# Optimization experiments

Hardware: AMD Instinct MI355X
Metric: run time of the kernel (lower is better)

The kernel has to match this reference:

```python
import jax, jax.numpy as jnp
import numpy as np

B, C, H, W = 4, 96, 64, 64
D_STATE, D_CONV, EXPAND = 16, 4, 2
D_INNER = EXPAND * C          # 192
DT_RANK = (C + 15) // 16      # 6
BN_EPS = 1e-5


def setup_inputs() -> dict:
    key = jax.random.key(0)
    ks = jax.random.split(key, 10)
    s = 0.02
    return {
        "x": jax.random.normal(ks[0], (B, C, H, W), jnp.float32),
        # Mamba block params (mamba_ssm layout, no bias on in/out proj)
        "in_proj_w": jax.random.normal(ks[1], (2 * D_INNER, C), jnp.float32) * s,
        "conv1d_w": jax.random.normal(ks[2], (D_INNER, 1, D_CONV), jnp.float32) * s,  # depthwise
        "conv1d_b": jnp.zeros((D_INNER,), jnp.float32),
        "x_proj_w": jax.random.normal(ks[3], (DT_RANK + 2 * D_STATE, D_INNER), jnp.float32) * s,
        "dt_proj_w": jax.random.normal(ks[4], (D_INNER, DT_RANK), jnp.float32) * s,
        "dt_proj_b": jax.random.normal(ks[5], (D_INNER,), jnp.float32) * s,
        "A_log": jnp.log(jnp.tile(jnp.arange(1, D_STATE + 1, dtype=jnp.float32), (D_INNER, 1))),
        "D": jnp.ones((D_INNER,), jnp.float32),
        "out_proj_w": jax.random.normal(ks[6], (C, D_INNER), jnp.float32) * s,
        # trailing ConvBNReLU6 params
        "conv2d_w": jax.random.normal(ks[7], (C, C, 3, 3), jnp.float32) * s,
        "bn_gamma": jnp.ones((C,), jnp.float32),
        "bn_beta": jnp.zeros((C,), jnp.float32),
        "bn_mean": jnp.zeros((C,), jnp.float32),
        "bn_var": jnp.ones((C,), jnp.float32),
    }


def _forward(x, in_proj_w, conv1d_w, conv1d_b, x_proj_w, dt_proj_w, dt_proj_b,
             A_log, D, out_proj_w, conv2d_w, bn_gamma, bn_beta, bn_mean, bn_var):
    b, c, h, w = x.shape
    L = h * w
    seq = x.reshape(b, c, L).transpose(0, 2, 1)              # [B, L, C] tokens
    xz = seq @ in_proj_w.T                                    # [B, L, 2*D_INNER]
    xi, z = jnp.split(xz, 2, axis=-1)

    # depthwise causal conv1d + SiLU
    xi_c = jax.lax.conv_general_dilated(
        xi.transpose(0, 2, 1), conv1d_w, (1,), [(D_CONV - 1, 0)],
        dimension_numbers=("NCH", "OIH", "NCH"), feature_group_count=D_INNER)
    xi = jax.nn.silu((xi_c + conv1d_b[None, :, None]).transpose(0, 2, 1))  # [B, L, D_INNER]

    # input-dependent dt, B, C
    x_dbl = xi @ x_proj_w.T                                   # [B, L, DT_RANK + 2*D_STATE]
    dt, Bm, Cm = jnp.split(x_dbl, [DT_RANK, DT_RANK + D_STATE], axis=-1)
    dt = jax.nn.softplus(dt @ dt_proj_w.T + dt_proj_b)        # [B, L, D_INNER]

    # discretize: dA = exp(dt*A), dBx = dt*B*x
    A = -jnp.exp(A_log)                                       # [D_INNER, D_STATE]
    dA = jnp.exp(dt[..., None] * A)                           # [B, L, D_INNER, D_STATE]
    dBx = dt[..., None] * Bm[:, :, None, :] * xi[..., None]   # [B, L, D_INNER, D_STATE]

    def step(hst, inputs):
        dA_t, dBx_t, C_t = inputs
        hst = dA_t * hst + dBx_t                              # [B, D_INNER, D_STATE]
        y_t = jnp.einsum("bds,bs->bd", hst, C_t)
        return hst, y_t

    h0 = jnp.zeros((b, D_INNER, D_STATE), xi.dtype)
    _, ys = jax.lax.scan(step, h0,
                         (dA.transpose(1, 0, 2, 3), dBx.transpose(1, 0, 2, 3), Cm.transpose(1, 0, 2)))
    y = ys.transpose(1, 0, 2)                                 # [B, L, D_INNER]
    y = (y + xi * D) * jax.nn.silu(z)                         # skip D + gate
    out = y @ out_proj_w.T                                    # [B, L, C]
    xm = out.transpose(0, 2, 1).reshape(b, c, h, w)

    # ConvBNReLU: 3x3 conv (pad 1, no bias) -> BN (inference) -> ReLU6
    xo = jax.lax.conv_general_dilated(xm, conv2d_w, (1, 1), [(1, 1), (1, 1)],
                                      dimension_numbers=("NCHW", "OIHW", "NCHW"))
    inv = bn_gamma / jnp.sqrt(bn_var + BN_EPS)
    xo = xo * inv[None, :, None, None] + (bn_beta - bn_mean * inv)[None, :, None, None]
    return jnp.clip(xo, 0.0, 6.0)


def reference(x, in_proj_w, conv1d_w, conv1d_b, x_proj_w, dt_proj_w, dt_proj_b,
              A_log, D, out_proj_w, conv2d_w, bn_gamma, bn_beta, bn_mean, bn_var):
    return _forward(x, in_proj_w, conv1d_w, conv1d_b, x_proj_w, dt_proj_w, dt_proj_b,
                    A_log, D, out_proj_w, conv2d_w, bn_gamma, bn_beta, bn_mean, bn_var)
```

## Files before the change

### kernel.cpp

```cpp
#include <hip/hip_runtime.h>
#include <math.h>

#define LQ 4096
#define DI 192
#define DS 16
#define NCH 256
#define TCH 16

__device__ __forceinline__ float siluf_(float v) { return v / (1.f + __expf(-v)); }
__device__ __forceinline__ float softplusf_(float v) { return v > 20.f ? v : log1pf(__expf(v)); }

template <int CTRL>
__device__ __forceinline__ float dpp_shift_(float x) {
    int y = __builtin_amdgcn_update_dpp(0, __float_as_int(x), CTRL, 0xf, 0xf, true);
    return __int_as_float(y);
}
__device__ __forceinline__ void async_g2l16_(const float* g, float* l) {
    __builtin_amdgcn_global_load_lds(
        (const __attribute__((address_space(1))) void*)g,
        (__attribute__((address_space(3))) void*)l, 16, 0, 0);
}
__device__ __forceinline__ void async_g2l4_(const float* g, float* l) {
    __builtin_amdgcn_global_load_lds(
        (const __attribute__((address_space(1))) void*)g,
        (__attribute__((address_space(3))) void*)l, 4, 0, 0);
}

__global__ __launch_bounds__(256) void k1_inproj(const float* __restrict__ x,
    const float* __restrict__ w, float* __restrict__ xi_raw, float* __restrict__ z)
{
    const int l0 = blockIdx.x * 64;
    const int n0 = blockIdx.y * 64;
    const int b  = blockIdx.z;
    __shared__ float xs[96 * 64];
    __shared__ float wsT[96 * 68];
    const int tid = threadIdx.x;
    for (int i = tid; i < 96 * 16; i += 256) {
        int c = i >> 4, lq = i & 15;
        *(float4*)&xs[c * 64 + lq * 4] =
            *(const float4*)&x[(b * 96 + c) * LQ + l0 + lq * 4];
    }
    for (int i = tid; i < 64 * 24; i += 256) {
        int n = i / 24, cq = i - n * 24;
        float4 v = *(const float4*)&w[(n0 + n) * 96 + cq * 4];
        wsT[(cq * 4 + 0) * 68 + n] = v.x;
        wsT[(cq * 4 + 1) * 68 + n] = v.y;
        wsT[(cq * 4 + 2) * 68 + n] = v.z;
        wsT[(cq * 4 + 3) * 68 + n] = v.w;
    }
    __syncthreads();
    const int tx = tid & 15;
    const int ty = tid >> 4;
    float acc[4][4];
#pragma unroll
    for (int i = 0; i < 4; ++i)
#pragma unroll
        for (int j = 0; j < 4; ++j) acc[i][j] = 0.f;
    for (int k = 0; k < 96; ++k) {
        float4 a  = *(const float4*)&xs[k * 64 + ty * 4];
        float4 bb = *(const float4*)&wsT[k * 68 + tx * 4];
        float av[4] = {a.x, a.y, a.z, a.w};
        float bv[4] = {bb.x, bb.y, bb.z, bb.w};
#pragma unroll
        for (int i = 0; i < 4; ++i)
#pragma unroll
            for (int j = 0; j < 4; ++j) acc[i][j] += av[i] * bv[j];
    }
    float* dst = (n0 < DI) ? xi_raw : z;
    const int nn0 = (n0 < DI) ? n0 : (n0 - DI);
#pragma unroll
    for (int i = 0; i < 4; ++i) {
        int l = l0 + ty * 4 + i;
        float4 v = make_float4(acc[i][0], acc[i][1], acc[i][2], acc[i][3]);
        *(float4*)&dst[(b * LQ + l) * DI + nn0 + tx * 4] = v;
    }
}

__global__ __launch_bounds__(256) void k2_conv1d(const float* __restrict__ xir,
    const float* __restrict__ cw, const float* __restrict__ cb, float* __restrict__ xi)
{
    int idx = blockIdx.x * 256 + threadIdx.x;
    int d = idx % DI;
    int l = (idx / DI) & (LQ - 1);
    float4 wv = *(const float4*)&cw[d * 4];
    float wk[4] = {wv.x, wv.y, wv.z, wv.w};
    float acc = cb[d];
#pragma unroll
    for (int k = 0; k < 4; ++k) {
        int lp = l - 3 + k;
        if (lp >= 0) acc += wk[k] * xir[idx + (k - 3) * DI];
    }
    xi[idx] = siluf_(acc);
}

__global__ __launch_bounds__(256) void k3_xdbl(const float* __restrict__ xi,
    const float* __restrict__ xw, float* __restrict__ xdbl)
{
    const int l0 = blockIdx.x * 64;
    const int b  = blockIdx.y;
    __shared__ float sxiT[96 * 68];
    __shared__ float swx[38 * 196];
    const int tid = threadIdx.x;
    for (int i = tid; i < 38 * 48; i += 256) {
        int n = i / 48, kq = i - n * 48;
        *(float4*)&swx[n * 196 + kq * 4] = *(const float4*)&xw[n * 192 + kq * 4];
    }
    const int lq = tid & 15, ng = tid >> 4;
    float acc[3][4];
#pragma unroll
    for (int p = 0; p < 3; ++p)
#pragma unroll
        for (int i = 0; i < 4; ++i) acc[p][i] = 0.f;
    for (int half = 0; half < 2; ++half) {
        __syncthreads();
        for (int i = tid; i < 64 * 24; i += 256) {
            int l = i / 24, kq = i - l * 24;
            float4 v = *(const float4*)&xi[(b * LQ + l0 + l) * DI + half * 96 + kq * 4];
            sxiT[(kq * 4 + 0) * 68 + l] = v.x;
            sxiT[(kq * 4 + 1) * 68 + l] = v.y;
            sxiT[(kq * 4 + 2) * 68 + l] = v.z;
            sxiT[(kq * 4 + 3) * 68 + l] = v.w;
        }
        __syncthreads();
#pragma unroll
        for (int pass = 0; pass < 3; ++pass) {
            int n = pass * 16 + ng;
            if (n >= 38) continue;
            for (int k = 0; k < 96; ++k) {
                float4 a = *(const float4*)&sxiT[k * 68 + lq * 4];
                float bv = swx[n * 196 + half * 96 + k];
                acc[pass][0] += a.x * bv;
                acc[pass][1] += a.y * bv;
                acc[pass][2] += a.z * bv;
                acc[pass][3] += a.w * bv;
            }
        }
    }
#pragma unroll
    for (int pass = 0; pass < 3; ++pass) {
        int n = pass * 16 + ng;
        if (n >= 38) continue;
#pragma unroll
        for (int i = 0; i < 4; ++i)
            xdbl[(b * LQ + l0 + lq * 4 + i) * 38 + n] = acc[pass][i];
    }
}

__global__ __launch_bounds__(192) void k4_scanA(
    const float* __restrict__ xdbl, const float* __restrict__ xi,
    const float* __restrict__ dtw, const float* __restrict__ dtb,
    const float* __restrict__ alog,
    float* __restrict__ cA, float* __restrict__ cB)
{
    const int ch = blockIdx.x, b = blockIdx.y;
    const int t0 = ch * TCH;
    __shared__ float sxd[TCH * 48];
    const int d = threadIdx.x;
    for (int i = d; i < TCH * 38; i += 192) {
        int t = i / 38, cc = i - t * 38;
        int slot = cc + (cc >= 6 ? 2 : 0);
        sxd[t * 48 + slot] = xdbl[(b * LQ + t0 + t) * 38 + cc];
    }
    float dtw6[6];
#pragma unroll
    for (int r = 0; r < 6; ++r) dtw6[r] = dtw[d * 6 + r];
    const float dtbd = dtb[d];
    float Ads[16];
#pragma unroll
    for (int s = 0; s < 16; ++s) Ads[s] = -__expf(alog[d * 16 + s]);
    float a[16], hb[16];
#pragma unroll
    for (int s = 0; s < 16; ++s) { a[s] = 1.f; hb[s] = 0.f; }
    __syncthreads();
    float xiv_next = xi[(b * LQ + t0) * DI + d];
    for (int t = 0; t < TCH; ++t) {
        float xiv = xiv_next;
        if (t + 1 < TCH) xiv_next = xi[(b * LQ + t0 + t + 1) * DI + d];
        float acc = dtbd;
#pragma unroll
        for (int r = 0; r < 6; ++r) acc = fmaf(sxd[t * 48 + r], dtw6[r], acc);
        float dtv = softplusf_(acc);
        float dtxi = dtv * xiv;
        const float* Bp = &sxd[t * 48 + 8];
        float Bv[16];
#pragma unroll
        for (int q = 0; q < 4; ++q) {
            float4 v = *(const float4*)(Bp + q * 4);
            Bv[q * 4] = v.x; Bv[q * 4 + 1] = v.y; Bv[q * 4 + 2] = v.z; Bv[q * 4 + 3] = v.w;
        }
#pragma unroll
        for (int s = 0; s < 16; ++s) {
            float dA = __expf(dtv * Ads[s]);
            a[s] *= dA;
            hb[s] = fmaf(dA, hb[s], dtxi * Bv[s]);
        }
    }
    int o = ((b * NCH + ch) * DI + d) * 16;
#pragma unroll
    for (int s = 0; s < 16; s += 4) {
        *(float4*)&cA[o + s] = make_float4(a[s], a[s + 1], a[s + 2], a[s + 3]);
        *(float4*)&cB[o + s] = make_float4(hb[s], hb[s + 1], hb[s + 2], hb[s + 3]);
    }
}

__global__ __launch_bounds__(256) void k5_combine(const float* cA,
    const float* __restrict__ cB, float* hinit)
{
    int gid = blockIdx.x * 256 + threadIdx.x;
    int b = gid / 3072;
    int rem = gid - b * 3072;
    int base = b * (NCH * 3072) + rem;
    float h = 0.f;
#pragma unroll 8
    for (int c = 0; c < NCH; ++c) {
        int o = base + c * 3072;
        float av = cA[o];
        float bv = cB[o];
        hinit[o] = h;
        h = fmaf(av, h, bv);
    }
}

__global__ __launch_bounds__(192) void k6_scanC(
    const float* __restrict__ xdbl, const float* __restrict__ xi,
    const float* __restrict__ z, const float* __restrict__ dtw,
    const float* __restrict__ dtb, const float* __restrict__ alog,
    const float* __restrict__ Dp, const float* __restrict__ hinit,
    float* __restrict__ yg)
{
    const int ch = blockIdx.x, b = blockIdx.y;
    const int t0 = ch * TCH;
    __shared__ float sxd[TCH * 48];
    const int d = threadIdx.x;
    for (int i = d; i < TCH * 38; i += 192) {
        int t = i / 38, cc = i - t * 38;
        int slot = cc + (cc >= 6 ? 2 : 0);
        sxd[t * 48 + slot] = xdbl[(b * LQ + t0 + t) * 38 + cc];
    }
    float dtw6[6];
#pragma unroll
    for (int r = 0; r < 6; ++r) dtw6[r] = dtw[d * 6 + r];
    const float dtbd = dtb[d];
    const float Dd = Dp[d];
    float Ads[16];
#pragma unroll
    for (int s = 0; s < 16; ++s) Ads[s] = -__expf(alog[d * 16 + s]);
    float h[16];
    const int o = ((b * NCH + ch) * DI + d) * 16;
#pragma unroll
    for (int s = 0; s < 16; s += 4) {
        float4 v = *(const float4*)&hinit[o + s];
        h[s] = v.x; h[s + 1] = v.y; h[s + 2] = v.z; h[s + 3] = v.w;
    }
    __syncthreads();
    float xiv_next = xi[(b * LQ + t0) * DI + d];
    float zv_next  = z[(b * LQ + t0) * DI + d];
    for (int t = 0; t < TCH; ++t) {
        float xiv = xiv_next, zv = zv_next;
        if (t + 1 < TCH) {
            xiv_next = xi[(b * LQ + t0 + t + 1) * DI + d];
            zv_next  = z[(b * LQ + t0 + t + 1) * DI + d];
        }
        float acc = dtbd;
#pragma unroll
        for (int r = 0; r < 6; ++r) acc = fmaf(sxd[t * 48 + r], dtw6[r], acc);
        float dtv = softplusf_(acc);
        float dtxi = dtv * xiv;
        const float* Bp = &sxd[t * 48 + 8];
        const float* Cp = &sxd[t * 48 + 24];
        float Bv[16], Cv[16];
#pragma unroll
        for (int q = 0; q < 4; ++q) {
            float4 vb = *(const float4*)(Bp + q * 4);
            float4 vc = *(const float4*)(Cp + q * 4);
            Bv[q * 4] = vb.x; Bv[q * 4 + 1] = vb.y; Bv[q * 4 + 2] = vb.z; Bv[q * 4 + 3] = vb.w;
            Cv[q * 4] = vc.x; Cv[q * 4 + 1] = vc.y; Cv[q * 4 + 2] = vc.z; Cv[q * 4 + 3] = vc.w;
        }
        float y0 = 0.f, y1 = 0.f, y2 = 0.f, y3 = 0.f;
#pragma unroll
        for (int s = 0; s < 16; s += 4) {
            float dA0 = __expf(dtv * Ads[s]);
            float dA1 = __expf(dtv * Ads[s + 1]);
            float dA2 = __expf(dtv * Ads[s + 2]);
            float dA3 = __expf(dtv * Ads[s + 3]);
            h[s]     = fmaf(dA0, h[s],     dtxi * Bv[s]);
            h[s + 1] = fmaf(dA1, h[s + 1], dtxi * Bv[s + 1]);
            h[s + 2] = fmaf(dA2, h[s + 2], dtxi * Bv[s + 2]);
            h[s + 3] = fmaf(dA3, h[s + 3], dtxi * Bv[s + 3]);
            y0 = fmaf(h[s],     Cv[s],     y0);
            y1 = fmaf(h[s + 1], Cv[s + 1], y1);
            y2 = fmaf(h[s + 2], Cv[s + 2], y2);
            y3 = fmaf(h[s + 3], Cv[s + 3], y3);
        }
        float y = (y0 + y1) + (y2 + y3);
        float gate = siluf_(zv);
        yg[(b * LQ + t0 + t) * DI + d] = (y + xiv * Dd) * gate;
    }
}

__global__ __launch_bounds__(256) void k7_outproj(const float* __restrict__ yg,
    const float* __restrict__ wo, float* __restrict__ xm)
{
    const int l0 = blockIdx.x * 64;
    const int n0 = blockIdx.y * 32;
    const int b  = blockIdx.z;
    __shared__ float syT[96 * 68];
    __shared__ float wtT[192 * 36];
    const int tid = threadIdx.x;
    for (int i = tid; i < 32 * 48; i += 256) {
        int n = i / 48, kq = i - n * 48;
        float4 v = *(const float4*)&wo[(n0 + n) * DI + kq * 4];
        wtT[(kq * 4 + 0) * 36 + n] = v.x;
        wtT[(kq * 4 + 1) * 36 + n] = v.y;
        wtT[(kq * 4 + 2) * 36 + n] = v.z;
        wtT[(kq * 4 + 3) * 36 + n] = v.w;
    }
    const int tx = tid & 15;
    const int ty = tid >> 4;
    float acc[2][4];
#pragma unroll
    for (int j = 0; j < 2; ++j)
#pragma unroll
        for (int i = 0; i < 4; ++i) acc[j][i] = 0.f;
    for (int half = 0; half < 2; ++half) {
        __syncthreads();
        for (int i = tid; i < 64 * 24; i += 256) {
            int l = i / 24, kq = i - l * 24;
            float4 v = *(const float4*)&yg[(b * LQ + l0 + l) * DI + half * 96 + kq * 4];
            syT[(kq * 4 + 0) * 68 + l] = v.x;
            syT[(kq * 4 + 1) * 68 + l] = v.y;
            syT[(kq * 4 + 2) * 68 + l] = v.z;
            syT[(kq * 4 + 3) * 68 + l] = v.w;
        }
        __syncthreads();
        for (int k = 0; k < 96; ++k) {
            float4 a = *(const float4*)&syT[k * 68 + tx * 4];
            int kk = half * 96 + k;
            float b0 = wtT[kk * 36 + ty * 2 + 0];
            float b1 = wtT[kk * 36 + ty * 2 + 1];
            acc[0][0] += a.x * b0; acc[0][1] += a.y * b0;
            acc[0][2] += a.z * b0; acc[0][3] += a.w * b0;
            acc[1][0] += a.x * b1; acc[1][1] += a.y * b1;
            acc[1][2] += a.z * b1; acc[1][3] += a.w * b1;
        }
    }
#pragma unroll
    for (int j = 0; j < 2; ++j) {
        float4 v = make_float4(acc[j][0], acc[j][1], acc[j][2], acc[j][3]);
        *(float4*)&xm[(b * 96 + n0 + ty * 2 + j) * LQ + l0 + tx * 4] = v;
    }
}

#define K8_INQ 384
#define K8_WNEL 576
__global__ __launch_bounds__(256) void k8_conv3(const float* __restrict__ xm,
    const float* __restrict__ w2, float* __restrict__ pbuf)
{
    const int ks  = blockIdx.x & 3;
    const int co0 = (blockIdx.x >> 2) * 16;
    const int y0  = blockIdx.y * 4;
    const int b   = blockIdx.z;
    __shared__ float sin2[2][1536];
    __shared__ float swt2[2][576];
    const int tid = threadIdx.x;
    const int sx = tid & 15;
    const int sy = (tid >> 4) & 3;
    const int cq = tid >> 6;

    int in_goff[2];
    bool in_ok[2];
#pragma unroll
    for (int j = 0; j < 2; ++j) {
        int i = tid + j * 256;
        int ci  = i / 96;
        int rem = i - ci * 96;
        int row = rem >> 4;
        int qx  = rem & 15;
        int gy  = y0 + row - 1;
        bool ok = (i < K8_INQ) && gy >= 0 && gy < 64;
        in_ok[j]  = ok;
        in_goff[j] = ok ? (ci * 4096 + gy * 64 + qx * 4) : 0;
    }
    int w_goff[3];
#pragma unroll
    for (int j = 0; j < 3; ++j) {
        int i = tid + j * 256;
        int ci  = i / 144;
        int rem = i - ci * 144;
        int k   = rem >> 4;
        int cl  = rem & 15;
        w_goff[j] = (i < K8_WNEL) ? (cl * 864 + ci * 9 + k) : 0;
    }

    const float* xb = xm + (size_t)b * 96 * 4096 + (size_t)ks * 24 * 4096;
    const float* wb = w2 + (size_t)co0 * 864 + ks * 24 * 9;
    const float4 zero4 = make_float4(0.f, 0.f, 0.f, 0.f);

#pragma unroll
    for (int bu = 0; bu < 2; ++bu) {
        if (!in_ok[0]) *(float4*)&sin2[bu][tid * 4] = zero4;
        if (tid < 128 && !in_ok[1]) *(float4*)&sin2[bu][(256 + tid) * 4] = zero4;
    }

    {
        const float* gx = xb;
        const float* gw = wb;
        if (in_ok[0]) async_g2l16_(gx + in_goff[0], &sin2[0][cq * 256]);
        if (tid < 128 && in_ok[1]) async_g2l16_(gx + in_goff[1], &sin2[0][1024 + cq * 256]);
        async_g2l4_(gw + w_goff[0], &swt2[0][cq * 64]);
        async_g2l4_(gw + w_goff[1], &swt2[0][256 + cq * 64]);
        if (tid < 64) async_g2l4_(gw + w_goff[2], &swt2[0][512 + cq * 64]);
    }
    __syncthreads();

    float acc[4][4];
#pragma unroll
    for (int c = 0; c < 4; ++c)
#pragma unroll
        for (int x = 0; x < 4; ++x) acc[c][x] = 0.f;

#pragma clang loop unroll(disable)
    for (int ch = 0; ch < 6; ++ch) {
        if (ch < 5) {
            const int nb = (ch + 1) & 1;
            const float* gx = xb + (ch + 1) * 16384;
            const float* gw = wb + (ch + 1) * 36;
            if (in_ok[0]) async_g2l16_(gx + in_goff[0], &sin2[nb][cq * 256]);
            if (tid < 128 && in_ok[1]) async_g2l16_(gx + in_goff[1], &sin2[nb][1024 + cq * 256]);
            async_g2l4_(gw + w_goff[0], &swt2[nb][cq * 64]);
            async_g2l4_(gw + w_goff[1], &swt2[nb][256 + cq * 64]);
            if (tid < 64) async_g2l4_(gw + w_goff[2], &swt2[nb][512 + cq * 64]);
        }

        const float* sc = sin2[ch & 1];
        const float* wc = swt2[ch & 1];
#pragma unroll
        for (int cii = 0; cii < 4; ++cii) {
            float w6[3][6];
#pragma unroll
            for (int r = 0; r < 3; ++r) {
                float4 v = *(const float4*)&sc[(cii * 6 + sy + r) * 64 + sx * 4];
                w6[r][0] = dpp_shift_<0x111>(v.w);
                w6[r][1] = v.x; w6[r][2] = v.y; w6[r][3] = v.z; w6[r][4] = v.w;
                w6[r][5] = dpp_shift_<0x101>(v.x);
            }
#pragma unroll
            for (int ky = 0; ky < 3; ++ky) {
#pragma unroll
                for (int kx = 0; kx < 3; ++kx) {
                    float4 wv = *(const float4*)&wc[(cii * 9 + ky * 3 + kx) * 16 + cq * 4];
#pragma unroll
                    for (int x = 0; x < 4; ++x) {
                        float pv = w6[ky][x + kx];
                        acc[0][x] = fmaf(pv, wv.x, acc[0][x]);
                        acc[1][x] = fmaf(pv, wv.y, acc[1][x]);
                        acc[2][x] = fmaf(pv, wv.z, acc[2][x]);
                        acc[3][x] = fmaf(pv, wv.w, acc[3][x]);
                    }
                }
            }
        }
        __syncthreads();
    }

    const int yy = y0 + sy;
    float* pb = pbuf + (size_t)ks * 1572864;
#pragma unroll
    for (int c = 0; c < 4; ++c) {
        const int cc = co0 + cq * 4 + c;
        float4 o = make_float4(acc[c][0], acc[c][1], acc[c][2], acc[c][3]);
        *(float4*)&pb[((size_t)(b * 96 + cc) * 64 + yy) * 64 + sx * 4] = o;
    }
}

__global__ __launch_bounds__(256) void k9_reduce(const float* __restrict__ pbuf,
    const float* __restrict__ bng, const float* __restrict__ bnb,
    const float* __restrict__ bnm, const float* __restrict__ bnv,
    float* __restrict__ out)
{
    const int q = blockIdx.x * 256 + threadIdx.x;
    const int idx = q * 4;
    const int c = (idx >> 12) % 96;
    float4 s = *(const float4*)&pbuf[idx];
    float4 s1 = *(const float4*)&pbuf[idx + 1572864];
    float4 s2 = *(const float4*)&pbuf[idx + 2 * 1572864];
    float4 s3 = *(const float4*)&pbuf[idx + 3 * 1572864];
    s.x += s1.x + s2.x + s3.x;
    s.y += s1.y + s2.y + s3.y;
    s.z += s1.z + s2.z + s3.z;
    s.w += s1.w + s2.w + s3.w;
    float inv = bng[c] / sqrtf(bnv[c] + 1e-5f);
    float add = bnb[c] - bnm[c] * inv;
    float4 o;
    o.x = fminf(fmaxf(s.x * inv + add, 0.f), 6.f);
    o.y = fminf(fmaxf(s.y * inv + add, 0.f), 6.f);
    o.z = fminf(fmaxf(s.z * inv + add, 0.f), 6.f);
    o.w = fminf(fmaxf(s.w * inv + add, 0.f), 6.f);
    *(float4*)&out[idx] = o;
}

extern "C" void kernel_launch(void* const* d_in, const int* in_sizes, int n_in,
                              void* d_out, int out_size, void* d_ws, size_t ws_size,
                              hipStream_t stream) {
    (void)in_sizes; (void)n_in; (void)out_size; (void)ws_size;
    const float* x    = (const float*)d_in[0];
    const float* w_in = (const float*)d_in[1];
    const float* cw   = (const float*)d_in[2];
    const float* cb   = (const float*)d_in[3];
    const float* xw   = (const float*)d_in[4];
    const float* dtw  = (const float*)d_in[5];
    const float* dtb  = (const float*)d_in[6];
    const float* alog = (const float*)d_in[7];
    const float* Dp   = (const float*)d_in[8];
    const float* wo   = (const float*)d_in[9];
    const float* w2   = (const float*)d_in[10];
    const float* bng  = (const float*)d_in[11];
    const float* bnb  = (const float*)d_in[12];
    const float* bnm  = (const float*)d_in[13];
    const float* bnv  = (const float*)d_in[14];

    float* ws = (float*)d_ws;
    float* xi_raw = ws;
    float* z      = ws + 3145728;
    float* xi     = ws + 6291456;
    float* xdbl   = ws + 9437184;
    float* cA     = ws + 10059776;
    float* cB     = xi_raw;
    float* hinit  = cA;
    float* yg     = xi_raw;
    float* xm     = cA;
    float* pbuf   = z;

    dim3 blk(256);
    k1_inproj<<<dim3(64, 6, 4), blk, 0, stream>>>(x, w_in, xi_raw, z);
    k2_conv1d<<<dim3(12288), blk, 0, stream>>>(xi_raw, cw, cb, xi);
    k3_xdbl<<<dim3(64, 4), blk, 0, stream>>>(xi, xw, xdbl);
    k4_scanA<<<dim3(NCH, 4), dim3(192), 0, stream>>>(xdbl, xi, dtw, dtb, alog, cA, cB);
    k5_combine<<<dim3(48), blk, 0, stream>>>(cA, cB, hinit);
    k6_scanC<<<dim3(NCH, 4), dim3(192), 0, stream>>>(xdbl, xi, z, dtw, dtb, alog, Dp, hinit, yg);
    k7_outproj<<<dim3(64, 3, 4), blk, 0, stream>>>(yg, wo, xm);
    k8_conv3<<<dim3(24, 16, 4), blk, 0, stream>>>(xm, w2, pbuf);
    k9_reduce<<<dim3(1536), blk, 0, stream>>>(pbuf, bng, bnb, bnm, bnv, (float*)d_out);
}
```

Baseline: 296.2 us.

## Parallelize chunk scan over state dimension and precompute dt in shared memory

The chunk-summary scan kernel now assigns one thread per (channel, state) pair instead of one thread per channel looping over 16 states. Each block covers 16 channels and precomputes softplus(dt) for its tile into shared memory, together with the xi slice. The chunk count is halved and the chunk length doubled, which also changes the combine and scan-C kernels through NCH/TCH. Workspace aliasing is rearranged so cB gets its own region, and xm and pbuf move to other buffers. This trades more parallelism and lower register pressure for more blocks and extra shared-memory staging, with a longer sequential combine-free chunk in k6.

```diff
diff --git a/kernel.cpp b/kernel.cpp
--- a/kernel.cpp
+++ b/kernel.cpp
@@ -4,8 +4,8 @@
 #define LQ 4096
 #define DI 192
 #define DS 16
-#define NCH 256
-#define TCH 16
+#define NCH 128
+#define TCH 32
 
 __device__ __forceinline__ float siluf_(float v) { return v / (1.f + __expf(-v)); }
 __device__ __forceinline__ float softplusf_(float v) { return v > 20.f ? v : log1pf(__expf(v)); }
@@ -146,61 +146,51 @@
     }
 }
 
-__global__ __launch_bounds__(192) void k4_scanA(
+__global__ __launch_bounds__(256) void k4_scanA(
     const float* __restrict__ xdbl, const float* __restrict__ xi,
     const float* __restrict__ dtw, const float* __restrict__ dtb,
     const float* __restrict__ alog,
     float* __restrict__ cA, float* __restrict__ cB)
 {
-    const int ch = blockIdx.x, b = blockIdx.y;
-    const int t0 = ch * TCH;
-    __shared__ float sxd[TCH * 48];
-    const int d = threadIdx.x;
-    for (int i = d; i < TCH * 38; i += 192) {
+    const int ch = blockIdx.x, g = blockIdx.y, b = blockIdx.z;
+    const int t0 = ch * TCH, d0 = g * 16;
+    __shared__ float sxd[TCH * 40];
+    __shared__ float sdt[TCH * 16], sxi[TCH * 16];
+    __shared__ float sdtw[96], sdtb[16];
+    const int tid = threadIdx.x;
+    for (int i = tid; i < TCH * 38; i += 256) {
         int t = i / 38, cc = i - t * 38;
-        int slot = cc + (cc >= 6 ? 2 : 0);
-        sxd[t * 48 + slot] = xdbl[(b * LQ + t0 + t) * 38 + cc];
-    }
-    float dtw6[6];
-#pragma unroll
-    for (int r = 0; r < 6; ++r) dtw6[r] = dtw[d * 6 + r];
-    const float dtbd = dtb[d];
-    float Ads[16];
-#pragma unroll
-    for (int s = 0; s < 16; ++s) Ads[s] = -__expf(alog[d * 16 + s]);
-    float a[16], hb[16];
-#pragma unroll
-    for (int s = 0; s < 16; ++s) { a[s] = 1.f; hb[s] = 0.f; }
+        sxd[t * 40 + cc] = xdbl[(b * LQ + t0 + t) * 38 + cc];
+    }
+    for (int i = tid; i < TCH * 16; i += 256) {
+        int t = i >> 4, j = i & 15;
+        sxi[i] = xi[(b * LQ + t0 + t) * DI + d0 + j];
+    }
+    if (tid < 96) sdtw[tid] = dtw[d0 * 6 + tid];
+    if (tid < 16) sdtb[tid] = dtb[d0 + tid];
     __syncthreads();
-    float xiv_next = xi[(b * LQ + t0) * DI + d];
+    for (int i = tid; i < TCH * 16; i += 256) {
+        int t = i >> 4, dl = i & 15;
+        float acc = sdtb[dl];
+#pragma unroll
+        for (int r = 0; r < 6; ++r) acc += sxd[t * 40 + r] * sdtw[dl * 6 + r];
+        sdt[i] = softplusf_(acc);
+    }
+    __syncthreads();
+    const int s = tid & 15, dl = tid >> 4;
+    const float Ads = -__expf(alog[(d0 + dl) * DS + s]);
+    float a = 1.f, hb = 0.f;
+#pragma unroll 4
     for (int t = 0; t < TCH; ++t) {
-        float xiv = xiv_next;
-        if (t + 1 < TCH) xiv_next = xi[(b * LQ + t0 + t + 1) * DI + d];
-        float acc = dtbd;
-#pragma unroll
-        for (int r = 0; r < 6; ++r) acc = fmaf(sxd[t * 48 + r], dtw6[r], acc);
-        float dtv = softplusf_(acc);
-        float dtxi = dtv * xiv;
-        const float* Bp = &sxd[t * 48 + 8];
-        float Bv[16];
-#pragma unroll
-        for (int q = 0; q < 4; ++q) {
-            float4 v = *(const float4*)(Bp + q * 4);
-            Bv[q * 4] = v.x; Bv[q * 4 + 1] = v.y; Bv[q * 4 + 2] = v.z; Bv[q * 4 + 3] = v.w;
-        }
-#pragma unroll
-        for (int s = 0; s < 16; ++s) {
-            float dA = __expf(dtv * Ads[s]);
-            a[s] *= dA;
-            hb[s] = fmaf(dA, hb[s], dtxi * Bv[s]);
-        }
-    }
-    int o = ((b * NCH + ch) * DI + d) * 16;
-#pragma unroll
-    for (int s = 0; s < 16; s += 4) {
-        *(float4*)&cA[o + s] = make_float4(a[s], a[s + 1], a[s + 2], a[s + 3]);
-        *(float4*)&cB[o + s] = make_float4(hb[s], hb[s + 1], hb[s + 2], hb[s + 3]);
-    }
+        float dtv = sdt[t * 16 + dl];
+        float dA = __expf(dtv * Ads);
+        float dbx = dtv * sxd[t * 40 + 6 + s] * sxi[t * 16 + dl];
+        a *= dA;
+        hb = dA * hb + dbx;
+    }
+    int o = ((b * NCH + ch) * DI + d0 + dl) * DS + s;
+    cA[o] = a;
+    cB[o] = hb;
 }
 
 __global__ __launch_bounds__(256) void k5_combine(const float* cA,
@@ -525,17 +515,17 @@
     float* xi     = ws + 6291456;
     float* xdbl   = ws + 9437184;
     float* cA     = ws + 10059776;
-    float* cB     = xi_raw;
+    float* cB     = ws + 11632640;
     float* hinit  = cA;
+    float* xm     = cB;
     float* yg     = xi_raw;
-    float* xm     = cA;
-    float* pbuf   = z;
+    float* pbuf   = xi_raw;
 
     dim3 blk(256);
     k1_inproj<<<dim3(64, 6, 4), blk, 0, stream>>>(x, w_in, xi_raw, z);
     k2_conv1d<<<dim3(12288), blk, 0, stream>>>(xi_raw, cw, cb, xi);
     k3_xdbl<<<dim3(64, 4), blk, 0, stream>>>(xi, xw, xdbl);
-    k4_scanA<<<dim3(NCH, 4), dim3(192), 0, stream>>>(xdbl, xi, dtw, dtb, alog, cA, cB);
+    k4_scanA<<<dim3(NCH, 12, 4), blk, 0, stream>>>(xdbl, xi, dtw, dtb, alog, cA, cB);
     k5_combine<<<dim3(48), blk, 0, stream>>>(cA, cB, hinit);
     k6_scanC<<<dim3(NCH, 4), dim3(192), 0, stream>>>(xdbl, xi, z, dtw, dtb, alog, Dp, hinit, yg);
     k7_outproj<<<dim3(64, 3, 4), blk, 0, stream>>>(yg, wo, xm);
```

Result: faster. 283.4 us (-4.3%).
